# Performance work log

Measured on AMD Instinct MI355X. Metric: run time of the kernel, lower is better.

Reference implementation:

```python
import jax, jax.numpy as jnp
import numpy as np

N_NODES = 10000
N_EDGES = 40000
N_GRAPHS = 64
NODE_DIM = 64
EDGE_DIM = 16
HIDDEN = 64
LAYERS = 3


def setup_inputs() -> dict:
    key = jax.random.key(0)
    ks = jax.random.split(key, 20)
    s = 0.05
    inp = {
        "x": jax.random.normal(ks[0], (N_NODES, NODE_DIM), jnp.float32),
        "edge_attr": jax.random.normal(ks[1], (N_EDGES, EDGE_DIM), jnp.float32),
        "edge_index": jax.random.randint(ks[2], (2, N_EDGES), 0, N_NODES),
        "batch": jnp.sort(jax.random.randint(ks[3], (N_NODES,), 0, N_GRAPHS)),
        # input projection
        "proj_w": jax.random.normal(ks[4], (NODE_DIM, HIDDEN), jnp.float32) * s,
        "proj_b": jnp.zeros((HIDDEN,), jnp.float32),
        # per-layer EdgeMLP: edge_dim -> hidden -> hidden*hidden
        "edge_w1": jax.random.normal(ks[5], (LAYERS, EDGE_DIM, HIDDEN), jnp.float32) * s,
        "edge_b1": jnp.zeros((LAYERS, HIDDEN), jnp.float32),
        "edge_w2": jax.random.normal(ks[6], (LAYERS, HIDDEN, HIDDEN * HIDDEN), jnp.float32) * s,
        "edge_b2": jnp.zeros((LAYERS, HIDDEN * HIDDEN), jnp.float32),
        # per-layer NNConv root weight + bias
        "root_w": jax.random.normal(ks[7], (LAYERS, HIDDEN, HIDDEN), jnp.float32) * s,
        "conv_b": jnp.zeros((LAYERS, HIDDEN), jnp.float32),
        # head MLP: hidden -> hidden -> 1
        "head_w1": jax.random.normal(ks[8], (HIDDEN, HIDDEN), jnp.float32) * s,
        "head_b1": jnp.zeros((HIDDEN,), jnp.float32),
        "head_w2": jax.random.normal(ks[9], (HIDDEN, 1), jnp.float32) * s,
        "head_b2": jnp.zeros((1,), jnp.float32),
    }
    return inp


def reference(x, edge_attr, edge_index, batch, proj_w, proj_b,
              edge_w1, edge_b1, edge_w2, edge_b2, root_w, conv_b,
              head_w1, head_b1, head_w2, head_b2):
    n = x.shape[0]
    src, dst = edge_index[0], edge_index[1]  # messages flow src -> dst

    # in-degree at destination for mean aggregation (0 for isolated nodes)
    deg = jax.ops.segment_sum(jnp.ones_like(src, dtype=x.dtype), dst, num_segments=n)
    inv_deg = jnp.where(deg > 0, 1.0 / jnp.maximum(deg, 1.0), 0.0)

    h = x @ proj_w + proj_b  # [N, H]
    for l in range(LAYERS):
        # edge-conditioned weight: [E, H, H]
        theta = jax.nn.silu(edge_attr @ edge_w1[l] + edge_b1[l]) @ edge_w2[l] + edge_b2[l]
        theta = theta.reshape(-1, HIDDEN, HIDDEN)
        # per-edge matmul of gathered source features
        msg = jnp.einsum('ei,eio->eo', h[src], theta)  # [E, H]
        agg = jax.ops.segment_sum(msg, dst, num_segments=n) * inv_deg[:, None]
        h = jax.nn.silu(agg + h @ root_w[l] + conv_b[l])

    # global mean pool over graphs
    gcnt = jax.ops.segment_sum(jnp.ones((n,), x.dtype), batch, num_segments=N_GRAPHS)
    hg = jax.ops.segment_sum(h, batch, num_segments=N_GRAPHS) / jnp.maximum(gcnt, 1.0)[:, None]

    out = jax.nn.silu(hg @ head_w1 + head_b1) @ head_w2 + head_b2  # [G, 1]
    return out.reshape(-1)
```

## Files before the change

### kernel.cpp

```cpp
#include <hip/hip_runtime.h>
#include <math.h>

#define NN 10000
#define NE 40000
#define NGRAPH 64
#define HID 64
#define EDIM 16
#define NLAYERS 3

#define NRT 625
#define NCT 260
#define WFRAG 512
#define PWL ((size_t)NCT * 2 * 3 * WFRAG)

#define GN 16
#define KPAD 68
#define JSTR (16 * KPAD + 4)

typedef __attribute__((ext_vector_type(8))) short bf8v;
typedef __attribute__((ext_vector_type(4))) float f32x4;

__device__ __forceinline__ float silu_f(float x) { return x / (1.f + expf(-x)); }

__device__ __forceinline__ unsigned short f2bf(float f) {
    unsigned int u = __float_as_uint(f);
    u += 0x7fff + ((u >> 16) & 1);
    return (unsigned short)(u >> 16);
}
__device__ __forceinline__ float bf2f(unsigned short s) {
    return __uint_as_float(((unsigned int)s) << 16);
}
__device__ __forceinline__ void split3f(float v, short& a, short& b, short& c) {
    unsigned short u1 = f2bf(v);      float f1 = bf2f(u1);
    unsigned short u2 = f2bf(v - f1); float f2 = bf2f(u2);
    unsigned short u3 = f2bf(v - f1 - f2);
    a = (short)u1; b = (short)u2; c = (short)u3;
}

template<int K, bool DO_SILU, bool HAS_BIAS>
__global__ __launch_bounds__(256)
void k_rowmm(const float* __restrict__ A, const float* __restrict__ W,
             const float* __restrict__ bias, float* __restrict__ out, int M) {
    __shared__ float Ws[K * 64];
    __shared__ float As[4 * K];
    const int tid = threadIdx.x;
    for (int idx = tid; idx < K * 64; idx += 256) Ws[idx] = W[idx];
    const int r0 = blockIdx.x * 4;
    for (int idx = tid; idx < 4 * K; idx += 256) {
        int r = r0 + idx / K;
        As[idx] = (r < M) ? A[(size_t)r * K + (idx % K)] : 0.f;
    }
    __syncthreads();
    const int rr = tid >> 6, c = tid & 63;
    const int r = r0 + rr;
    if (r >= M) return;
    float s = HAS_BIAS ? bias[c] : 0.f;
#pragma unroll
    for (int k = 0; k < K; k++) s += As[rr * K + k] * Ws[k * 64 + c];
    if (DO_SILU) s = silu_f(s);
    out[(size_t)r * 64 + c] = s;
}

__global__ __launch_bounds__(256)
void k_gmm3(const float* __restrict__ ea, const float* __restrict__ ew1,
            const float* __restrict__ eb1, float* __restrict__ g3) {
    const int l = blockIdx.y;
    const float* W = ew1 + (size_t)l * EDIM * 64;
    const float* bias = eb1 + (size_t)l * 64;
    float* out = g3 + (size_t)l * NE * 64;
    __shared__ float Ws[EDIM * 64];
    __shared__ float As[4 * EDIM];
    const int tid = threadIdx.x;
    for (int idx = tid; idx < EDIM * 64; idx += 256) Ws[idx] = W[idx];
    const int r0 = blockIdx.x * 4;
    if (tid < 4 * EDIM) As[tid] = ea[(size_t)r0 * EDIM + tid];
    __syncthreads();
    const int rr = tid >> 6, c = tid & 63;
    float s = bias[c];
#pragma unroll
    for (int k = 0; k < EDIM; k++) s += As[rr * EDIM + k] * Ws[k * 64 + c];
    out[(size_t)(r0 + rr) * 64 + c] = silu_f(s);
}

__global__ void k_hist(const int* __restrict__ ei, int* __restrict__ cnt_s,
                       int* __restrict__ cnt_d) {
    int e = blockIdx.x * 256 + threadIdx.x;
    if (e >= NE) return;
    atomicAdd(&cnt_s[ei[e]], 1);
    atomicAdd(&cnt_d[ei[NE + e]], 1);
}

__global__ __launch_bounds__(1024)
void k_scan2(const int* __restrict__ cnt_s, const int* __restrict__ cnt_d,
             int* __restrict__ off_s, int* __restrict__ off_d,
             int* __restrict__ cur_s, int* __restrict__ cur_d,
             float* __restrict__ invd) {
    __shared__ int part[1024];
    const int t = threadIdx.x;
    const int CH = (NN + 1023) / 1024;
    const int base0 = t * CH;
#pragma unroll
    for (int pass = 0; pass < 2; ++pass) {
        const int* cnt = pass ? cnt_d : cnt_s;
        int* off = pass ? off_d : off_s;
        int* cur = pass ? cur_d : cur_s;
        int s = 0;
        for (int i = 0; i < CH; i++) {
            int idx = base0 + i;
            if (idx < NN) s += cnt[idx];
        }
        part[t] = s;
        __syncthreads();
        for (int d = 1; d < 1024; d <<= 1) {
            int v = (t >= d) ? part[t - d] : 0;
            __syncthreads();
            part[t] += v;
            __syncthreads();
        }
        int run = (t == 0) ? 0 : part[t - 1];
        for (int i = 0; i < CH; i++) {
            int idx = base0 + i;
            if (idx < NN) {
                off[idx] = run;
                int c = cnt[idx];
                if (pass) invd[idx] = (c > 0) ? 1.f / (float)c : 0.f;
                run += c;
                cur[idx] = 0;
            }
        }
        if (t == 1023) off[NN] = run;
        __syncthreads();
    }
}

__global__ void k_fill(const int* __restrict__ keys, const int* __restrict__ off,
                       int* __restrict__ cur, int* __restrict__ eid) {
    int e = blockIdx.x * 256 + threadIdx.x;
    if (e >= NE) return;
    int s = keys[e];
    int p = atomicAdd(&cur[s], 1);
    eid[off[s] + p] = e;
}

__global__ __launch_bounds__(128)
void k_packw(const float* __restrict__ ew2, const float* __restrict__ eb2,
             short* __restrict__ pw) {
    const int ct = blockIdx.x;
    const int lay = blockIdx.y;
    const int t = threadIdx.x;
    const int l = t & 63, ks = t >> 6;
    const int col = ct * 16 + (l & 15);
    const int i0 = ks * 32 + ((l >> 4) << 3);
    bf8v v1, v2, v3;
#pragma unroll
    for (int tt = 0; tt < 8; ++tt) {
        const int i = i0 + tt;
        float v;
        if (col < 4096)
            v = ew2[(size_t)lay * 262144 + (size_t)(col >> 6) * 4096 + i * 64 + (col & 63)];
        else
            v = eb2[(size_t)lay * 4096 + i * 64 + (col - 4096)];
        short a, b, c;
        split3f(v, a, b, c);
        v1[tt] = a; v2[tt] = b; v3[tt] = c;
    }
    short* dst = pw + ((((size_t)lay * NCT + ct) * 2 + ks) * 3) * WFRAG + l * 8;
    *reinterpret_cast<bf8v*>(dst)        = v1;
    *reinterpret_cast<bf8v*>(dst + 512)  = v2;
    *reinterpret_cast<bf8v*>(dst + 1024) = v3;
}

__global__ __launch_bounds__(128)
void k_packh(const float* __restrict__ h, short* __restrict__ ph) {
    const int rt = blockIdx.x;
    const int t = threadIdx.x;
    const int l = t & 63, ks = t >> 6;
    const int row = rt * 16 + (l & 15);
    const int i0 = ks * 32 + ((l >> 4) << 3);
    const float* hp = h + (size_t)row * 64 + i0;
    bf8v v1, v2, v3;
#pragma unroll
    for (int tt = 0; tt < 8; ++tt) {
        short a, b, c;
        split3f(hp[tt], a, b, c);
        v1[tt] = a; v2[tt] = b; v3[tt] = c;
    }
    short* dst = ph + (((size_t)rt * 2 + ks) * 3) * WFRAG + l * 8;
    *reinterpret_cast<bf8v*>(dst)        = v1;
    *reinterpret_cast<bf8v*>(dst + 512)  = v2;
    *reinterpret_cast<bf8v*>(dst + 1024) = v3;
}

__global__ __launch_bounds__(512, 4)
void k_msgfused(const short* __restrict__ ph, const short* __restrict__ pw,
                const float* __restrict__ g, const int* __restrict__ csr_off,
                const int* __restrict__ csr_eid, float* __restrict__ msg) {
    __shared__ float Bt[16 * JSTR];
    __shared__ float C_s[16 * 16];
    __shared__ int offs[GN + 1];

    const int grp = blockIdx.x, q = blockIdx.y;
    const int lane = threadIdx.x & 63;
    const int wid  = threadIdx.x >> 6;

    if (threadIdx.x <= GN) offs[threadIdx.x] = csr_off[grp * GN + threadIdx.x];

    bf8v A[2][3];
#pragma unroll
    for (int ks = 0; ks < 2; ++ks)
#pragma unroll
        for (int sp = 0; sp < 3; ++sp)
            A[ks][sp] = *reinterpret_cast<const bf8v*>(
                ph + (((size_t)grp * 2 + ks) * 3 + sp) * WFRAG + lane * 8);

    const int oq_w = lane & 15;
    const int jb   = (lane >> 4) << 2;

#pragma unroll 4
    for (int kk = 0; kk < 8; ++kk) {
        const int k = wid * 8 + kk;
        const int ct = k * 4 + q;
        bf8v Bf[2][3];
#pragma unroll
        for (int ks = 0; ks < 2; ++ks)
#pragma unroll
            for (int sp = 0; sp < 3; ++sp)
                Bf[ks][sp] = *reinterpret_cast<const bf8v*>(
                    pw + (((size_t)ct * 2 + ks) * 3 + sp) * WFRAG + lane * 8);
        f32x4 acc = {0.f, 0.f, 0.f, 0.f};
#pragma unroll
        for (int ks = 0; ks < 2; ++ks) {
            acc = __builtin_amdgcn_mfma_f32_16x16x32_bf16(A[ks][0], Bf[ks][0], acc, 0, 0, 0);
            acc = __builtin_amdgcn_mfma_f32_16x16x32_bf16(A[ks][0], Bf[ks][1], acc, 0, 0, 0);
            acc = __builtin_amdgcn_mfma_f32_16x16x32_bf16(A[ks][1], Bf[ks][0], acc, 0, 0, 0);
            acc = __builtin_amdgcn_mfma_f32_16x16x32_bf16(A[ks][0], Bf[ks][2], acc, 0, 0, 0);
            acc = __builtin_amdgcn_mfma_f32_16x16x32_bf16(A[ks][1], Bf[ks][1], acc, 0, 0, 0);
            acc = __builtin_amdgcn_mfma_f32_16x16x32_bf16(A[ks][2], Bf[ks][0], acc, 0, 0, 0);
        }
#pragma unroll
        for (int r = 0; r < 4; ++r)
            Bt[(jb + r) * JSTR + oq_w * KPAD + k] = acc[r];
    }
    if (wid == 7) {
        const int ct = 256 + q;
        bf8v Bf[2][3];
#pragma unroll
        for (int ks = 0; ks < 2; ++ks)
#pragma unroll
            for (int sp = 0; sp < 3; ++sp)
                Bf[ks][sp] = *reinterpret_cast<const bf8v*>(
                    pw + (((size_t)ct * 2 + ks) * 3 + sp) * WFRAG + lane * 8);
        f32x4 acc = {0.f, 0.f, 0.f, 0.f};
#pragma unroll
        for (int ks = 0; ks < 2; ++ks) {
            acc = __builtin_amdgcn_mfma_f32_16x16x32_bf16(A[ks][0], Bf[ks][0], acc, 0, 0, 0);
            acc = __builtin_amdgcn_mfma_f32_16x16x32_bf16(A[ks][0], Bf[ks][1], acc, 0, 0, 0);
            acc = __builtin_amdgcn_mfma_f32_16x16x32_bf16(A[ks][1], Bf[ks][0], acc, 0, 0, 0);
            acc = __builtin_amdgcn_mfma_f32_16x16x32_bf16(A[ks][0], Bf[ks][2], acc, 0, 0, 0);
            acc = __builtin_amdgcn_mfma_f32_16x16x32_bf16(A[ks][1], Bf[ks][1], acc, 0, 0, 0);
            acc = __builtin_amdgcn_mfma_f32_16x16x32_bf16(A[ks][2], Bf[ks][0], acc, 0, 0, 0);
        }
#pragma unroll
        for (int r = 0; r < 4; ++r)
            C_s[(jb + r) * 16 + oq_w] = acc[r];
    }
    __syncthreads();

    const int P0 = offs[0];
    const int Etot = offs[GN] - P0;
    const int oq = threadIdx.x & 15;
    const int eq = threadIdx.x >> 4;
    for (int slot = eq; slot < Etot; slot += 32) {
        const int gpos = P0 + slot;
        int j = 0;
#pragma unroll
        for (int t = 1; t < GN; ++t) j += (gpos >= offs[t]) ? 1 : 0;
        const int e = csr_eid[gpos];
        const float* grow = g + (size_t)e * 64;
        const float* Bj = Bt + j * JSTR + oq * KPAD;
        float m = C_s[j * 16 + oq];
#pragma unroll
        for (int k4 = 0; k4 < 16; ++k4) {
            const float4 gv = *(const float4*)(grow + k4 * 4);
            const float4 bv = *(const float4*)(Bj + k4 * 4);
            m += gv.x * bv.x + gv.y * bv.y + gv.z * bv.z + gv.w * bv.w;
        }
        msg[(size_t)e * 64 + q * 16 + oq] = m;
    }
}

__global__ __launch_bounds__(256)
void k_aggfin(const float* __restrict__ h, const float* __restrict__ msg,
              const int* __restrict__ off2, const int* __restrict__ eid2,
              const float* __restrict__ invd, const float* __restrict__ rw,
              const float* __restrict__ cb, float* __restrict__ hout) {
    __shared__ float Ws[64 * 64];
    __shared__ float As[8 * 64];
    __shared__ int eoff[9];
    const int tid = threadIdx.x;
    for (int idx = tid; idx < 64 * 64; idx += 256) Ws[idx] = rw[idx];
    const int r0 = blockIdx.x * 8;
    for (int idx = tid; idx < 8 * 64; idx += 256) As[idx] = h[(size_t)r0 * 64 + idx];
    if (tid < 9) eoff[tid] = off2[r0 + tid];
    __syncthreads();
    const int rr = tid >> 6, c = tid & 63;
#pragma unroll
    for (int half = 0; half < 2; ++half) {
        const int lr = half * 4 + rr;
        const int r = r0 + lr;
        float a = 0.f;
        for (int p = eoff[lr]; p < eoff[lr + 1]; ++p) {
            a += msg[(size_t)eid2[p] * 64 + c];
        }
        float s = cb[c] + a * invd[r];
        const float* Ar = As + lr * 64;
#pragma unroll
        for (int k = 0; k < 64; k++) s += Ar[k] * Ws[k * 64 + c];
        hout[(size_t)r * 64 + c] = silu_f(s);
    }
}

__global__ __launch_bounds__(256)
void k_poolhead(const float* __restrict__ h, const int* __restrict__ batch,
                const float* __restrict__ w1, const float* __restrict__ b1,
                const float* __restrict__ w2, const float* __restrict__ b2,
                float* __restrict__ out) {
    __shared__ float part[4 * 64];
    __shared__ float hrow[64];
    const int gidx = blockIdx.x;
    const int tid = threadIdx.x;
    const int r = tid >> 6, o = tid & 63;
    int lo = 0, hi = NN;
    while (lo < hi) { int m = (lo + hi) >> 1; if (batch[m] < gidx) lo = m + 1; else hi = m; }
    const int beg = lo;
    hi = NN;
    while (lo < hi) { int m = (lo + hi) >> 1; if (batch[m] < gidx + 1) lo = m + 1; else hi = m; }
    const int end = lo;
    float acc = 0.f;
    for (int n = beg + r; n < end; n += 4) acc += h[(size_t)n * 64 + o];
    part[r * 64 + o] = acc;
    __syncthreads();
    if (tid < 64) {
        const int cnt = end - beg;
        const float inv = (cnt > 0) ? 1.f / (float)cnt : 1.f;
        hrow[tid] = (part[tid] + part[64 + tid] + part[128 + tid] + part[192 + tid]) * inv;
    }
    __syncthreads();
    if (tid < 64) {
        float s = b1[tid];
#pragma unroll
        for (int k = 0; k < 64; ++k) s += hrow[k] * w1[k * 64 + tid];
        s = silu_f(s);
        float v = s * w2[tid];
#pragma unroll
        for (int d = 32; d > 0; d >>= 1) v += __shfl_down(v, d);
        if (tid == 0) out[gidx] = v + b2[0];
    }
}

extern "C" void kernel_launch(void* const* d_in, const int* in_sizes, int n_in,
                              void* d_out, int out_size, void* d_ws, size_t ws_size,
                              hipStream_t stream) {
    const float* x     = (const float*)d_in[0];
    const float* ea    = (const float*)d_in[1];
    const int*   ei    = (const int*)  d_in[2];
    const int*   batch = (const int*)  d_in[3];
    const float* pw    = (const float*)d_in[4];
    const float* pb    = (const float*)d_in[5];
    const float* ew1   = (const float*)d_in[6];
    const float* eb1   = (const float*)d_in[7];
    const float* ew2   = (const float*)d_in[8];
    const float* eb2   = (const float*)d_in[9];
    const float* rw    = (const float*)d_in[10];
    const float* cb    = (const float*)d_in[11];
    const float* hw1   = (const float*)d_in[12];
    const float* hb1   = (const float*)d_in[13];
    const float* hw2   = (const float*)d_in[14];
    const float* hb2   = (const float*)d_in[15];
    float* out = (float*)d_out;

    float* ws = (float*)d_ws;
    size_t off = 0;
    auto alloc = [&](size_t n) {
        float* p = ws + off;
        off += (n + 63) & ~(size_t)63;
        return p;
    };
    float* hA   = alloc((size_t)NN * 64);
    float* hBuf = alloc((size_t)NN * 64);
    float* msg  = alloc((size_t)NE * 64);
    float* invd = alloc(NN);
    int* off_s = (int*)alloc(NN + 1);
    int* off_d = (int*)alloc(NN + 1);
    int* cnt_s = (int*)alloc(NN);
    int* cnt_d = (int*)alloc(NN);
    int* cur_s = (int*)alloc(NN);
    int* cur_d = (int*)alloc(NN);
    int* eid_s = (int*)alloc(NE);
    int* eid_d = (int*)alloc(NE);
    short* packW = (short*)alloc(3 * PWL / 2 + 64);
    short* packH = (short*)alloc((size_t)NRT * 2 * 3 * WFRAG / 2 + 64);

    const size_t needG3 = (size_t)3 * NE * 64;
    bool batchG = (off + needG3 + 128) * sizeof(float) <= ws_size;
    float* gbuf = alloc(batchG ? needG3 : (size_t)NE * 64);

    hipMemsetAsync(cnt_s, 0, NN * sizeof(int), stream);
    hipMemsetAsync(cnt_d, 0, NN * sizeof(int), stream);

    k_hist<<<dim3((NE + 255) / 256), dim3(256), 0, stream>>>(ei, cnt_s, cnt_d);
    k_scan2<<<dim3(1), dim3(1024), 0, stream>>>(cnt_s, cnt_d, off_s, off_d,
                                                cur_s, cur_d, invd);
    k_fill<<<dim3((NE + 255) / 256), dim3(256), 0, stream>>>(ei, off_s, cur_s, eid_s);
    k_fill<<<dim3((NE + 255) / 256), dim3(256), 0, stream>>>(ei + NE, off_d, cur_d, eid_d);

    k_packw<<<dim3(NCT, 3), dim3(128), 0, stream>>>(ew2, eb2, packW);

    k_rowmm<64, false, true><<<dim3(NN / 4), dim3(256), 0, stream>>>(x, pw, pb, hA, NN);

    if (batchG) {
        k_gmm3<<<dim3(NE / 4, 3), dim3(256), 0, stream>>>(ea, ew1, eb1, gbuf);
    }

    float* hcur = hA;
    float* hnxt = hBuf;
    for (int l = 0; l < NLAYERS; l++) {
        float* gl = batchG ? gbuf + (size_t)l * NE * 64 : gbuf;
        if (!batchG) {
            k_rowmm<16, true, true><<<dim3(NE / 4), dim3(256), 0, stream>>>(
                ea, ew1 + (size_t)l * EDIM * 64, eb1 + (size_t)l * 64, gl, NE);
        }
        k_packh<<<dim3(NRT), dim3(128), 0, stream>>>(hcur, packH);
        k_msgfused<<<dim3(NRT, 4), dim3(512), 0, stream>>>(
            packH, packW + (size_t)l * PWL, gl, off_s, eid_s, msg);
        k_aggfin<<<dim3(NN / 8), dim3(256), 0, stream>>>(
            hcur, msg, off_d, eid_d, invd, rw + (size_t)l * 64 * 64,
            cb + (size_t)l * 64, hnxt);
        float* t = hcur; hcur = hnxt; hnxt = t;
    }

    k_poolhead<<<dim3(NGRAPH), dim3(256), 0, stream>>>(
        hcur, batch, hw1, hb1, hw2, hb2, out);
}
```

Before: 349.1 us.

## Process two row tiles per block in fused message kernel with 1024 threads

```diff
diff --git a/kernel.cpp b/kernel.cpp
--- a/kernel.cpp
+++ b/kernel.cpp
@@ -13,9 +13,11 @@
 #define WFRAG 512
 #define PWL ((size_t)NCT * 2 * 3 * WFRAG)
 
-#define GN 16
+#define GN 32
+#define NGRP 313
 #define KPAD 68
 #define JSTR (16 * KPAD + 4)
+#define MSG_LDS_FLOATS (GN * JSTR + GN * 16)
 
 typedef __attribute__((ext_vector_type(8))) short bf8v;
 typedef __attribute__((ext_vector_type(4))) float f32x4;
@@ -191,34 +193,45 @@
     *reinterpret_cast<bf8v*>(dst + 1024) = v3;
 }
 
-__global__ __launch_bounds__(512, 4)
+__global__ __launch_bounds__(1024, 4)
 void k_msgfused(const short* __restrict__ ph, const short* __restrict__ pw,
                 const float* __restrict__ g, const int* __restrict__ csr_off,
                 const int* __restrict__ csr_eid, float* __restrict__ msg) {
-    __shared__ float Bt[16 * JSTR];
-    __shared__ float C_s[16 * 16];
+    extern __shared__ float lds[];
+    float* Bt  = lds;
+    float* C_s = lds + GN * JSTR;
     __shared__ int offs[GN + 1];
 
     const int grp = blockIdx.x, q = blockIdx.y;
     const int lane = threadIdx.x & 63;
     const int wid  = threadIdx.x >> 6;
 
-    if (threadIdx.x <= GN) offs[threadIdx.x] = csr_off[grp * GN + threadIdx.x];
-
-    bf8v A[2][3];
+    if (threadIdx.x <= GN) {
+        int idx = grp * GN + threadIdx.x;
+        offs[threadIdx.x] = csr_off[idx < NN ? idx : NN];
+    }
+
+    const int rt0 = grp * 2;
+    const bool ok1 = (rt0 + 1 < NRT);
+
+    bf8v A[2][2][3];
 #pragma unroll
     for (int ks = 0; ks < 2; ++ks)
 #pragma unroll
-        for (int sp = 0; sp < 3; ++sp)
-            A[ks][sp] = *reinterpret_cast<const bf8v*>(
-                ph + (((size_t)grp * 2 + ks) * 3 + sp) * WFRAG + lane * 8);
+        for (int sp = 0; sp < 3; ++sp) {
+            A[0][ks][sp] = *reinterpret_cast<const bf8v*>(
+                ph + (((size_t)rt0 * 2 + ks) * 3 + sp) * WFRAG + lane * 8);
+            if (ok1)
+                A[1][ks][sp] = *reinterpret_cast<const bf8v*>(
+                    ph + (((size_t)(rt0 + 1) * 2 + ks) * 3 + sp) * WFRAG + lane * 8);
+        }
 
     const int oq_w = lane & 15;
     const int jb   = (lane >> 4) << 2;
 
-#pragma unroll 4
-    for (int kk = 0; kk < 8; ++kk) {
-        const int k = wid * 8 + kk;
+#pragma unroll
+    for (int kk = 0; kk < 4; ++kk) {
+        const int k = wid * 4 + kk;
         const int ct = k * 4 + q;
         bf8v Bf[2][3];
 #pragma unroll
@@ -227,21 +240,24 @@
             for (int sp = 0; sp < 3; ++sp)
                 Bf[ks][sp] = *reinterpret_cast<const bf8v*>(
                     pw + (((size_t)ct * 2 + ks) * 3 + sp) * WFRAG + lane * 8);
-        f32x4 acc = {0.f, 0.f, 0.f, 0.f};
+        f32x4 acc0 = {0.f, 0.f, 0.f, 0.f};
+        f32x4 acc1 = {0.f, 0.f, 0.f, 0.f};
 #pragma unroll
         for (int ks = 0; ks < 2; ++ks) {
-            acc = __builtin_amdgcn_mfma_f32_16x16x32_bf16(A[ks][0], Bf[ks][0], acc, 0, 0, 0);
-            acc = __builtin_amdgcn_mfma_f32_16x16x32_bf16(A[ks][0], Bf[ks][1], acc, 0, 0, 0);
-            acc = __builtin_amdgcn_mfma_f32_16x16x32_bf16(A[ks][1], Bf[ks][0], acc, 0, 0, 0);
-            acc = __builtin_amdgcn_mfma_f32_16x16x32_bf16(A[ks][0], Bf[ks][2], acc, 0, 0, 0);
-            acc = __builtin_amdgcn_mfma_f32_16x16x32_bf16(A[ks][1], Bf[ks][1], acc, 0, 0, 0);
-            acc = __builtin_amdgcn_mfma_f32_16x16x32_bf16(A[ks][2], Bf[ks][0], acc, 0, 0, 0);
-        }
-#pragma unroll
-        for (int r = 0; r < 4; ++r)
-            Bt[(jb + r) * JSTR + oq_w * KPAD + k] = acc[r];
-    }
-    if (wid == 7) {
+#define TERM(s1, s2) \
+            acc0 = __builtin_amdgcn_mfma_f32_16x16x32_bf16(A[0][ks][s1], Bf[ks][s2], acc0, 0, 0, 0); \
+            if (ok1) acc1 = __builtin_amdgcn_mfma_f32_16x16x32_bf16(A[1][ks][s1], Bf[ks][s2], acc1, 0, 0, 0);
+            TERM(0, 0) TERM(0, 1) TERM(1, 0) TERM(0, 2) TERM(1, 1) TERM(2, 0)
+#undef TERM
+        }
+#pragma unroll
+        for (int r = 0; r < 4; ++r) {
+            Bt[(jb + r) * JSTR + oq_w * KPAD + k]        = acc0[r];
+            if (ok1)
+                Bt[(16 + jb + r) * JSTR + oq_w * KPAD + k] = acc1[r];
+        }
+    }
+    if (wid == 15) {
         const int ct = 256 + q;
         bf8v Bf[2][3];
 #pragma unroll
@@ -250,19 +266,21 @@
             for (int sp = 0; sp < 3; ++sp)
                 Bf[ks][sp] = *reinterpret_cast<const bf8v*>(
                     pw + (((size_t)ct * 2 + ks) * 3 + sp) * WFRAG + lane * 8);
-        f32x4 acc = {0.f, 0.f, 0.f, 0.f};
+        f32x4 acc0 = {0.f, 0.f, 0.f, 0.f};
+        f32x4 acc1 = {0.f, 0.f, 0.f, 0.f};
 #pragma unroll
         for (int ks = 0; ks < 2; ++ks) {
-            acc = __builtin_amdgcn_mfma_f32_16x16x32_bf16(A[ks][0], Bf[ks][0], acc, 0, 0, 0);
-            acc = __builtin_amdgcn_mfma_f32_16x16x32_bf16(A[ks][0], Bf[ks][1], acc, 0, 0, 0);
-            acc = __builtin_amdgcn_mfma_f32_16x16x32_bf16(A[ks][1], Bf[ks][0], acc, 0, 0, 0);
-            acc = __builtin_amdgcn_mfma_f32_16x16x32_bf16(A[ks][0], Bf[ks][2], acc, 0, 0, 0);
-            acc = __builtin_amdgcn_mfma_f32_16x16x32_bf16(A[ks][1], Bf[ks][1], acc, 0, 0, 0);
-            acc = __builtin_amdgcn_mfma_f32_16x16x32_bf16(A[ks][2], Bf[ks][0], acc, 0, 0, 0);
-        }
-#pragma unroll
-        for (int r = 0; r < 4; ++r)
-            C_s[(jb + r) * 16 + oq_w] = acc[r];
+#define TERM(s1, s2) \
+            acc0 = __builtin_amdgcn_mfma_f32_16x16x32_bf16(A[0][ks][s1], Bf[ks][s2], acc0, 0, 0, 0); \
+            if (ok1) acc1 = __builtin_amdgcn_mfma_f32_16x16x32_bf16(A[1][ks][s1], Bf[ks][s2], acc1, 0, 0, 0);
+            TERM(0, 0) TERM(0, 1) TERM(1, 0) TERM(0, 2) TERM(1, 1) TERM(2, 0)
+#undef TERM
+        }
+#pragma unroll
+        for (int r = 0; r < 4; ++r) {
+            C_s[(jb + r) * 16 + oq_w] = acc0[r];
+            if (ok1) C_s[(16 + jb + r) * 16 + oq_w] = acc1[r];
+        }
     }
     __syncthreads();
 
@@ -270,7 +288,7 @@
     const int Etot = offs[GN] - P0;
     const int oq = threadIdx.x & 15;
     const int eq = threadIdx.x >> 4;
-    for (int slot = eq; slot < Etot; slot += 32) {
+    for (int slot = eq; slot < Etot; slot += 64) {
         const int gpos = P0 + slot;
         int j = 0;
 #pragma unroll
@@ -405,6 +423,10 @@
     bool batchG = (off + needG3 + 128) * sizeof(float) <= ws_size;
     float* gbuf = alloc(batchG ? needG3 : (size_t)NE * 64);
 
+    const size_t MSG_LDS_BYTES = (size_t)MSG_LDS_FLOATS * sizeof(float);
+    hipFuncSetAttribute(reinterpret_cast<const void*>(k_msgfused),
+                        hipFuncAttributeMaxDynamicSharedMemorySize, (int)MSG_LDS_BYTES);
+
     hipMemsetAsync(cnt_s, 0, NN * sizeof(int), stream);
     hipMemsetAsync(cnt_d, 0, NN * sizeof(int), stream);
 
@@ -431,7 +453,7 @@
                 ea, ew1 + (size_t)l * EDIM * 64, eb1 + (size_t)l * 64, gl, NE);
         }
         k_packh<<<dim3(NRT), dim3(128), 0, stream>>>(hcur, packH);
-        k_msgfused<<<dim3(NRT, 4), dim3(512), 0, stream>>>(
+        k_msgfused<<<dim3(NGRP, 4), dim3(1024), MSG_LDS_BYTES, stream>>>(
             packH, packW + (size_t)l * PWL, gl, off_s, eid_s, msg);
         k_aggfin<<<dim3(NN / 8), dim3(256), 0, stream>>>(
             hcur, msg, off_d, eid_d, invd, rw + (size_t)l * 64 * 64,
```

New measurement: 492.7 us. 1.41x slower.
